# Kernel optimization log

Hardware: AMD Instinct MI355X
Metric: run time of the kernel (lower is better)

The kernel has to match this reference:

```python
import jax, jax.numpy as jnp
import numpy as np

H = 256   # hidden size
U = 10    # attention units


def _lstm_cell(xt, h, c, Wih, Whh, bih, bhh):
    # PyTorch gate order: i, f, g, o
    gates = xt @ Wih.T + h @ Whh.T + bih + bhh          # [B, 4H]
    i, f, g, o = jnp.split(gates, 4, axis=-1)
    i = jax.nn.sigmoid(i); f = jax.nn.sigmoid(f)
    g = jnp.tanh(g);       o = jax.nn.sigmoid(o)
    c = f * c + i * g
    h = o * jnp.tanh(c)
    return h, c


def setup_inputs() -> dict:
    key = jax.random.key(0)
    ks = jax.random.split(key, 12)
    B, S = 512, 256
    s = 1.0 / np.sqrt(H)
    x = jax.random.normal(ks[0], (B, S), dtype=jnp.float32)
    y = jax.random.randint(ks[1], (B, S), 0, S, dtype=jnp.int64)
    return {
        "x": x,
        "y": y,
        "enc_Wih": jax.random.uniform(ks[2], (4 * H, 1), jnp.float32, -s, s),
        "enc_Whh": jax.random.uniform(ks[3], (4 * H, H), jnp.float32, -s, s),
        "enc_bih": jax.random.uniform(ks[4], (4 * H,), jnp.float32, -s, s),
        "enc_bhh": jax.random.uniform(ks[5], (4 * H,), jnp.float32, -s, s),
        "dec_Wih": jax.random.uniform(ks[6], (4 * H, H + 1), jnp.float32, -s, s),
        "dec_Whh": jax.random.uniform(ks[7], (4 * H, H), jnp.float32, -s, s),
        "dec_bih": jax.random.uniform(ks[8], (4 * H,), jnp.float32, -s, s),
        "dec_bhh": jax.random.uniform(ks[9], (4 * H,), jnp.float32, -s, s),
        "att_W1": jax.random.uniform(ks[10], (U, H), jnp.float32, -s, s),
        "att_W2": jax.random.uniform(ks[11], (U, H), jnp.float32, -s, s),
        "att_V": jax.random.uniform(jax.random.fold_in(key, 99), (1, U), jnp.float32, -s, s),
    }


def reference(x, y, enc_Wih, enc_Whh, enc_bih, enc_bhh,
              dec_Wih, dec_Whh, dec_bih, dec_bhh,
              att_W1, att_W2, att_V):
    B, S = x.shape

    # ---- Encoder: LSTM over sequence of scalar inputs ----
    def enc_step(carry, xt):  # xt: [B, 1]
        h, c = carry
        h, c = _lstm_cell(xt, h, c, enc_Wih, enc_Whh, enc_bih, enc_bhh)
        return (h, c), h

    h0 = jnp.zeros((B, H), x.dtype)
    (hN, cN), enc_out_t = jax.lax.scan(enc_step, (h0, h0), x.T[:, :, None])
    enc_out = jnp.transpose(enc_out_t, (1, 0, 2))            # [B, S, H]

    # precompute W1 @ encoder_hidden (same math, hoisted out of loop)
    encW1 = jnp.einsum('bsh,uh->bsu', enc_out, att_W1)       # [B, S, U]

    # ---- Decoder loop (teacher forcing with ratio 1.0) ----
    def dec_step(carry, y_t):
        h, c, dec_in = carry                                  # dec_in: [B, 1]
        u = jnp.tanh(encW1 + (h @ att_W2.T)[:, None, :])      # [B, S, U]
        logits = jnp.einsum('bsu,ou->bso', u, att_V)[..., 0]  # [B, S]
        aj = jax.nn.softmax(logits, axis=1)
        di = jnp.einsum('bs,bsh->bh', aj, enc_out)            # [B, H]
        lstm_in = jnp.concatenate([di, dec_in], axis=1)       # [B, H+1]
        h, c = _lstm_cell(lstm_in, h, c, dec_Wih, dec_Whh, dec_bih, dec_bhh)
        pred = jnp.argmax(logits, axis=1)                     # [B]
        logp = jax.nn.log_softmax(logits, axis=1)
        loss_t = -jnp.mean(jnp.take_along_axis(logp, y_t[:, None], axis=1))
        dec_in_next = jnp.take_along_axis(x, y_t[:, None], axis=1)  # teacher force
        return (h, c, dec_in_next), (pred, loss_t)

    dec_in0 = jnp.zeros((B, 1), x.dtype)
    _, (preds, losses) = jax.lax.scan(dec_step, (hN, cN, dec_in0), y.T)
    outputs = preds[:, :, None].astype(jnp.int64)             # [S, B, 1]
    batch_loss = jnp.sum(losses) / B
    return outputs, batch_loss
```

## Files before the change

kernel.cpp:

```cpp
#include <hip/hip_runtime.h>
#include <cmath>

__device__ __forceinline__ double dexp_(double x) {
    x = fmin(fmax(x, -64.0), 64.0);
    double w = x * 1.4426950408889634;
    double n = rint(w);
    double u = (w - n) * 0.6931471805599453;
    double p = 1.0 + u * (1.0 + u * (0.5 + u * (1.6666666666666666e-01 +
               u * (4.1666666666666664e-02 + u * (8.3333333333333332e-03 +
               u * (1.3888888888888889e-03 + u * (1.9841269841269841e-04 +
               u * (2.4801587301587302e-05 + u * (2.7557319223985893e-06 +
               u * (2.7557319223985888e-07 + u * 2.5052108385441720e-08))))))))));
    return ldexp(p, (int)n);
}
__device__ __forceinline__ double dtanh_(double x) {
    double ax = fabs(x);
    double e = dexp_(2.0 * ax);
    double t = 1.0 - 2.0 / (e + 1.0);
    return copysign(t, x);
}
__device__ __forceinline__ double dsig_(double x) {
    return 1.0 / (1.0 + dexp_(-x));
}

__device__ __forceinline__ void fma_range(
    const float* __restrict__ wcol, int row0, const float* __restrict__ xsrc,
    int k_beg, int k_end, double& A0, double& A1, double& A2, double& A3)
{
    for (int k0 = k_beg; k0 < k_end; k0 += 8) {
        float4 w[8];
        #pragma unroll
        for (int i = 0; i < 8; ++i)
            w[i] = *(const float4*)&wcol[(row0 + k0 + i) * 1024];
        float4 xa = *(const float4*)&xsrc[k0];
        float4 xb = *(const float4*)&xsrc[k0 + 4];
        float xv[8] = {xa.x, xa.y, xa.z, xa.w, xb.x, xb.y, xb.z, xb.w};
        float s0 = 0.f, s1 = 0.f, s2 = 0.f, s3 = 0.f;
        #pragma unroll
        for (int i = 0; i < 8; ++i) {
            s0 = fmaf(w[i].x, xv[i], s0);
            s1 = fmaf(w[i].y, xv[i], s1);
            s2 = fmaf(w[i].z, xv[i], s2);
            s3 = fmaf(w[i].w, xv[i], s3);
        }
        A0 += (double)s0; A1 += (double)s1;
        A2 += (double)s2; A3 += (double)s3;
    }
}

__global__ __launch_bounds__(256) void prep_kernel(
    const float* __restrict__ eWih, const float* __restrict__ eWhh,
    const float* __restrict__ ebih, const float* __restrict__ ebhh,
    const float* __restrict__ dWih, const float* __restrict__ dWhh,
    const float* __restrict__ dbih, const float* __restrict__ dbhh,
    float* __restrict__ WencR, double* __restrict__ bencR,
    float* __restrict__ WdecR, double* __restrict__ bdecR)
{
    const int n_enc = 257 * 1024;
    const int n_dec = 513 * 1024;
    const int total = n_enc + n_dec + 2048;
    for (int idx = blockIdx.x * blockDim.x + threadIdx.x; idx < total;
         idx += gridDim.x * blockDim.x) {
        if (idx < n_enc) {
            int k = idx >> 10, c = idx & 1023;
            int j = c >> 2, g = c & 3, r = g * 256 + j;
            WencR[idx] = (k == 0) ? eWih[r] : eWhh[r * 256 + (k - 1)];
        } else if (idx < n_enc + n_dec) {
            int i2 = idx - n_enc;
            int k = i2 >> 10, c = i2 & 1023;
            int j = c >> 2, g = c & 3, r = g * 256 + j;
            WdecR[i2] = (k < 257) ? dWih[r * 257 + k] : dWhh[r * 256 + (k - 257)];
        } else {
            int c = idx - n_enc - n_dec;
            if (c < 1024) {
                int r = (c & 3) * 256 + (c >> 2);
                bencR[c] = (double)ebih[r] + (double)ebhh[r];
            } else {
                int c2 = c - 1024;
                int r = (c2 & 3) * 256 + (c2 >> 2);
                bdecR[c2] = (double)dbih[r] + (double)dbhh[r];
            }
        }
    }
}

__global__ __launch_bounds__(256, 2) void enc_fused_kernel(
    const float* __restrict__ x, const float* __restrict__ W,
    const double* __restrict__ bR, float* __restrict__ enc_out,
    float* __restrict__ c_st)
{
    __shared__ float h_lds[2][256];
    const int tid = threadIdx.x;
    const int j   = tid;
    const int b   = blockIdx.x;

    h_lds[0][j] = 0.0f;
    float c_f = 0.f;
    const double bi = bR[j * 4 + 0], bf = bR[j * 4 + 1];
    const double bg = bR[j * 4 + 2], bo = bR[j * 4 + 3];
    const float* wcol = W + j * 4;

    for (int t = 0; t < 256; ++t) {
        const int cur = t & 1, nxt = cur ^ 1;
        __syncthreads();

        double A0 = 0, A1 = 0, A2 = 0, A3 = 0;
        const float* hh = h_lds[cur];
        fma_range(wcol, 1, hh, 0, 256, A0, A1, A2, A3);
        {
            float4 w = *(const float4*)&wcol[0];
            float xv = x[b * 256 + t];
            A0 += (double)(w.x * xv); A1 += (double)(w.y * xv);
            A2 += (double)(w.z * xv); A3 += (double)(w.w * xv);
        }

        double iv = dsig_(A0 + bi);
        double fv = dsig_(A1 + bf);
        double gv = dtanh_(A2 + bg);
        double ov = dsig_(A3 + bo);
        double c = fv * (double)c_f + iv * gv;
        c_f = (float)c;
        float hv = (float)(ov * dtanh_(c));
        enc_out[(long)b * 65536 + t * 256 + j] = hv;
        h_lds[nxt][j] = hv;
    }

    c_st[(long)b * 256 + j] = c_f;
}

__global__ __launch_bounds__(256) void encW1_kernel(
    const float* __restrict__ enc_out, const float* __restrict__ W1,
    double* __restrict__ encW1d)
{
    __shared__ float sa[64][260];
    __shared__ float sw[10][257];
    const int tid = threadIdx.x;
    const int m0 = blockIdx.x * 64;
    #pragma unroll
    for (int i = 0; i < 16; ++i) {
        int idx = tid + i * 256;
        int row = idx >> 6;
        int c4 = (idx & 63) * 4;
        const float4 v = *(const float4*)&enc_out[(long)(m0 + row) * 256 + c4];
        *(float4*)&sa[row][c4] = v;
    }
    for (int i = tid; i < 2560; i += 256) sw[i >> 8][i & 255] = W1[i];
    __syncthreads();
    for (int o = tid; o < 640; o += 256) {
        int r = o / 10;
        int u = o - r * 10;
        double acc = 0.0;
        #pragma unroll 4
        for (int k = 0; k < 256; ++k)
            acc += (double)sa[r][k] * (double)sw[u][k];
        encW1d[(long)(m0 + r) * 10 + u] = acc;
    }
}

__global__ __launch_bounds__(256) void transpose_kernel(float* __restrict__ eo)
{
    __shared__ float ta[32][33], tb[32][33];
    const int tid = threadIdx.x;
    const int r   = tid >> 3;
    const int c4  = (tid & 7) * 4;
    float* base = eo + (long)blockIdx.x * 65536;

    for (int ti = 0; ti < 8; ++ti) {
        for (int tj = ti; tj < 8; ++tj) {
            float4 va = *(const float4*)&base[(ti * 32 + r) * 256 + tj * 32 + c4];
            ta[r][c4 + 0] = va.x; ta[r][c4 + 1] = va.y;
            ta[r][c4 + 2] = va.z; ta[r][c4 + 3] = va.w;
            if (tj > ti) {
                float4 vb = *(const float4*)&base[(tj * 32 + r) * 256 + ti * 32 + c4];
                tb[r][c4 + 0] = vb.x; tb[r][c4 + 1] = vb.y;
                tb[r][c4 + 2] = vb.z; tb[r][c4 + 3] = vb.w;
            }
            __syncthreads();
            {
                float4 w;
                w.x = ta[c4 + 0][r]; w.y = ta[c4 + 1][r];
                w.z = ta[c4 + 2][r]; w.w = ta[c4 + 3][r];
                *(float4*)&base[(tj * 32 + r) * 256 + ti * 32 + c4] = w;
            }
            if (tj > ti) {
                float4 w;
                w.x = tb[c4 + 0][r]; w.y = tb[c4 + 1][r];
                w.z = tb[c4 + 2][r]; w.w = tb[c4 + 3][r];
                *(float4*)&base[(ti * 32 + r) * 256 + tj * 32 + c4] = w;
            }
            __syncthreads();
        }
    }
}

__global__ __launch_bounds__(256, 2) void dec_fused_kernel(
    const double* __restrict__ encW1d, const float* __restrict__ enc_out,
    const float* __restrict__ W2, const float* __restrict__ V,
    const float* __restrict__ x, const int* __restrict__ y,
    const float* __restrict__ W, const double* __restrict__ bR,
    const float* __restrict__ c_init, float* __restrict__ logp_buf,
    float* __restrict__ out_pred)
{
    __shared__ double eW_lds[10][260];
    __shared__ float  W2_lds[10][256];
    __shared__ float h_lds[2][256];
    __shared__ float di_lds[256];
    __shared__ float e_lds[256];
    __shared__ float rcpZ_s;
    __shared__ float din_s;
    __shared__ double s_V[12];
    __shared__ double s_W2h[12];
    __shared__ double s_ld[256];
    __shared__ double s_red[4];
    __shared__ int s_redi[4];
    __shared__ double s_maxd;
    __shared__ int s_am;

    const int tid  = threadIdx.x;
    const int j    = tid;
    const int wid  = tid >> 6;
    const int lane = tid & 63;
    const int b    = blockIdx.x;

    if (tid < 10) s_V[tid] = (double)V[tid];
    for (int i = tid; i < 2560; i += 256) {
        int s = i / 10, u = i - s * 10;
        eW_lds[u][s] = encW1d[(long)b * 2560 + i];
        W2_lds[i >> 8][i & 255] = W2[i];
    }
    h_lds[0][j] = enc_out[(long)b * 65536 + j * 256 + 255];
    float c_f = c_init[(long)b * 256 + j];
    const double bi = bR[j * 4 + 0], bf = bR[j * 4 + 1];
    const double bg = bR[j * 4 + 2], bo = bR[j * 4 + 3];
    const float* wcol = W + j * 4;
    __syncthreads();

    for (int t = 0; t < 256; ++t) {
        const int cur = t & 1, nxt = cur ^ 1;
        const float* hh = h_lds[cur];

        for (int u = wid; u < 10; u += 4) {
            double p = 0.0;
            #pragma unroll
            for (int i = 0; i < 4; ++i) {
                int k = lane + i * 64;
                p += (double)W2_lds[u][k] * (double)hh[k];
            }
            #pragma unroll
            for (int off = 32; off >= 1; off >>= 1) p += __shfl_down(p, off, 64);
            if (lane == 0) s_W2h[u] = p;
        }
        __syncthreads();

        double l = 0.0;
        #pragma unroll
        for (int u = 0; u < 10; ++u) l += s_V[u] * dtanh_(eW_lds[u][j] + s_W2h[u]);
        s_ld[j] = l;

        {
            double v = l; int idx = j;
            #pragma unroll
            for (int off = 32; off >= 1; off >>= 1) {
                double v2 = __shfl_down(v, off, 64);
                int i2 = __shfl_down(idx, off, 64);
                if (v2 > v || (v2 == v && i2 < idx)) { v = v2; idx = i2; }
            }
            if (lane == 0) { s_red[wid] = v; s_redi[wid] = idx; }
        }
        __syncthreads();
        if (tid == 0) {
            double v = s_red[0]; int idx = s_redi[0];
            #pragma unroll
            for (int w2 = 1; w2 < 4; ++w2) {
                if (s_red[w2] > v || (s_red[w2] == v && s_redi[w2] < idx)) {
                    v = s_red[w2]; idx = s_redi[w2];
                }
            }
            s_maxd = v; s_am = idx;
        }
        __syncthreads();

        double e = dexp_(l - s_maxd);
        e_lds[j] = (float)e;
        {
            double v = e;
            #pragma unroll
            for (int off = 32; off >= 1; off >>= 1) v += __shfl_down(v, off, 64);
            if (lane == 0) s_red[wid] = v;
        }
        __syncthreads();
        if (tid == 0) {
            double Z = s_red[0] + s_red[1] + s_red[2] + s_red[3];
            rcpZ_s = (float)(1.0 / Z);
            out_pred[t * 512 + b] = (float)s_am;
            int yv = y[b * 256 + t];
            logp_buf[t * 512 + b] = (float)(s_ld[yv] - s_maxd - log(Z));
        } else if (tid == 1) {
            float dv = 0.0f;
            if (t > 0) { int yi = y[b * 256 + (t - 1)]; dv = x[b * 256 + yi]; }
            din_s = dv;
        }
        __syncthreads();

        {
            const float* ep = enc_out + (long)b * 65536 + j * 256;
            float acc0 = 0.f, acc1 = 0.f, acc2 = 0.f, acc3 = 0.f;
            for (int s2 = 0; s2 < 256; s2 += 4) {
                float4 v = *(const float4*)&ep[s2];
                acc0 += e_lds[s2 + 0] * v.x;
                acc1 += e_lds[s2 + 1] * v.y;
                acc2 += e_lds[s2 + 2] * v.z;
                acc3 += e_lds[s2 + 3] * v.w;
            }
            di_lds[j] = ((acc0 + acc1) + (acc2 + acc3)) * rcpZ_s;
        }
        __syncthreads();

        double A0 = 0, A1 = 0, A2 = 0, A3 = 0;

        fma_range(wcol, 0, di_lds, 0, 256, A0, A1, A2, A3);
        {
            float4 w = *(const float4*)&wcol[256 * 1024];
            float xv = din_s;
            A0 += (double)(w.x * xv); A1 += (double)(w.y * xv);
            A2 += (double)(w.z * xv); A3 += (double)(w.w * xv);
        }
        fma_range(wcol, 257, hh, 0, 256, A0, A1, A2, A3);

        double iv = dsig_(A0 + bi);
        double fv = dsig_(A1 + bf);
        double gv = dtanh_(A2 + bg);
        double ov = dsig_(A3 + bo);
        double c = fv * (double)c_f + iv * gv;
        c_f = (float)c;
        h_lds[nxt][j] = (float)(ov * dtanh_(c));
        __syncthreads();
    }
}

__global__ __launch_bounds__(256) void loss_kernel(
    const float* __restrict__ logp_buf, float* __restrict__ out)
{
    const int tid = threadIdx.x;
    double acc = 0.0;
    for (int i = tid; i < 131072; i += 256) acc += (double)logp_buf[i];
    __shared__ double s_red[4];
    const int wid = tid >> 6, lane = tid & 63;
    #pragma unroll
    for (int off = 32; off >= 1; off >>= 1) acc += __shfl_down(acc, off, 64);
    if (lane == 0) s_red[wid] = acc;
    __syncthreads();
    if (tid == 0) {
        out[131072] = (float)(-(s_red[0] + s_red[1] + s_red[2] + s_red[3])
                              / (512.0 * 512.0));
    }
}

extern "C" void kernel_launch(void* const* d_in, const int* in_sizes, int n_in,
                              void* d_out, int out_size, void* d_ws, size_t ws_size,
                              hipStream_t stream)
{
    const float* x    = (const float*)d_in[0];
    const int*   y    = (const int*)  d_in[1];
    const float* eWih = (const float*)d_in[2];
    const float* eWhh = (const float*)d_in[3];
    const float* ebih = (const float*)d_in[4];
    const float* ebhh = (const float*)d_in[5];
    const float* dWih = (const float*)d_in[6];
    const float* dWhh = (const float*)d_in[7];
    const float* dbih = (const float*)d_in[8];
    const float* dbhh = (const float*)d_in[9];
    const float* W1   = (const float*)d_in[10];
    const float* W2   = (const float*)d_in[11];
    const float* V    = (const float*)d_in[12];

    double* encW1d = (double*)d_ws;
    double* bencR  = encW1d + 1310720;
    double* bdecR  = bencR + 1024;
    float* enc_out = (float*)(bdecR + 1024);
    float* c_st    = enc_out + 33554432;
    float* hzero   = c_st + 131072;
    float* hd      = hzero + 131072;
    float* dibuf   = hd + 262144;
    float* logp    = dibuf + 131072;
    float* WencR   = logp + 131072;
    float* WdecR   = WencR + 263168;

    float* out = (float*)d_out;

    prep_kernel<<<512, 256, 0, stream>>>(eWih, eWhh, ebih, ebhh,
                                         dWih, dWhh, dbih, dbhh,
                                         WencR, bencR, WdecR, bdecR);

    enc_fused_kernel<<<512, 256, 0, stream>>>(x, WencR, bencR, enc_out, c_st);

    encW1_kernel<<<2048, 256, 0, stream>>>(enc_out, W1, encW1d);

    transpose_kernel<<<512, 256, 0, stream>>>(enc_out);

    dec_fused_kernel<<<512, 256, 0, stream>>>(encW1d, enc_out, W2, V, x, y,
                                              WdecR, bdecR, c_st, logp, out);

    loss_kernel<<<1, 256, 0, stream>>>(logp, out);
}
```

Measured before the change: 17.37 ms.

## Cut decoder block barriers and stagger second-wave block start times

```diff
diff --git a/kernel.cpp b/kernel.cpp
--- a/kernel.cpp
+++ b/kernel.cpp
@@ -46,6 +46,11 @@
         A0 += (double)s0; A1 += (double)s1;
         A2 += (double)s2; A3 += (double)s3;
     }
+}
+
+__device__ __forceinline__ void stagger_spin(long cycles) {
+    long t0 = clock64();
+    while (clock64() - t0 < cycles) {}
 }
 
 __global__ __launch_bounds__(256) void prep_kernel(
@@ -94,6 +99,8 @@
     const int j   = tid;
     const int b   = blockIdx.x;
 
+    if (b & 256) stagger_spin(12000);
+
     h_lds[0][j] = 0.0f;
     float c_f = 0.f;
     const double bi = bR[j * 4 + 0], bf = bR[j * 4 + 1];
@@ -206,21 +213,19 @@
     __shared__ float h_lds[2][256];
     __shared__ float di_lds[256];
     __shared__ float e_lds[256];
-    __shared__ float rcpZ_s;
-    __shared__ float din_s;
     __shared__ double s_V[12];
-    __shared__ double s_W2h[12];
     __shared__ double s_ld[256];
     __shared__ double s_red[4];
     __shared__ int s_redi[4];
-    __shared__ double s_maxd;
-    __shared__ int s_am;
+    __shared__ double s_red2[4];
 
     const int tid  = threadIdx.x;
     const int j    = tid;
     const int wid  = tid >> 6;
     const int lane = tid & 63;
     const int b    = blockIdx.x;
+
+    if (b & 256) stagger_spin(48000);
 
     if (tid < 10) s_V[tid] = (double)V[tid];
     for (int i = tid; i < 2560; i += 256) {
@@ -239,7 +244,9 @@
         const int cur = t & 1, nxt = cur ^ 1;
         const float* hh = h_lds[cur];
 
-        for (int u = wid; u < 10; u += 4) {
+        double w2h[10];
+        #pragma unroll
+        for (int u = 0; u < 10; ++u) {
             double p = 0.0;
             #pragma unroll
             for (int i = 0; i < 4; ++i) {
@@ -248,15 +255,13 @@
             }
             #pragma unroll
             for (int off = 32; off >= 1; off >>= 1) p += __shfl_down(p, off, 64);
-            if (lane == 0) s_W2h[u] = p;
-        }
-        __syncthreads();
+            w2h[u] = __shfl(p, 0, 64);
+        }
 
         double l = 0.0;
         #pragma unroll
-        for (int u = 0; u < 10; ++u) l += s_V[u] * dtanh_(eW_lds[u][j] + s_W2h[u]);
+        for (int u = 0; u < 10; ++u) l += s_V[u] * dtanh_(eW_lds[u][j] + w2h[u]);
         s_ld[j] = l;
-
         {
             double v = l; int idx = j;
             #pragma unroll
@@ -268,7 +273,9 @@
             if (lane == 0) { s_red[wid] = v; s_redi[wid] = idx; }
         }
         __syncthreads();
-        if (tid == 0) {
+
+        double maxd; int am;
+        {
             double v = s_red[0]; int idx = s_redi[0];
             #pragma unroll
             for (int w2 = 1; w2 < 4; ++w2) {
@@ -276,31 +283,27 @@
                     v = s_red[w2]; idx = s_redi[w2];
                 }
             }
-            s_maxd = v; s_am = idx;
-        }
-        __syncthreads();
-
-        double e = dexp_(l - s_maxd);
+            maxd = v; am = idx;
+        }
+        double e = dexp_(l - maxd);
         e_lds[j] = (float)e;
         {
             double v = e;
             #pragma unroll
             for (int off = 32; off >= 1; off >>= 1) v += __shfl_down(v, off, 64);
-            if (lane == 0) s_red[wid] = v;
+            if (lane == 0) s_red2[wid] = v;
         }
         __syncthreads();
+
+        const double Z = s_red2[0] + s_red2[1] + s_red2[2] + s_red2[3];
+        const float rcpZ = (float)(1.0 / Z);
         if (tid == 0) {
-            double Z = s_red[0] + s_red[1] + s_red[2] + s_red[3];
-            rcpZ_s = (float)(1.0 / Z);
-            out_pred[t * 512 + b] = (float)s_am;
+            out_pred[t * 512 + b] = (float)am;
             int yv = y[b * 256 + t];
-            logp_buf[t * 512 + b] = (float)(s_ld[yv] - s_maxd - log(Z));
-        } else if (tid == 1) {
-            float dv = 0.0f;
-            if (t > 0) { int yi = y[b * 256 + (t - 1)]; dv = x[b * 256 + yi]; }
-            din_s = dv;
-        }
-        __syncthreads();
+            logp_buf[t * 512 + b] = (float)(s_ld[yv] - maxd - log(Z));
+        }
+        float din = 0.0f;
+        if (t > 0) { int yi = y[b * 256 + (t - 1)]; din = x[b * 256 + yi]; }
 
         {
             const float* ep = enc_out + (long)b * 65536 + j * 256;
@@ -312,7 +315,7 @@
                 acc2 += e_lds[s2 + 2] * v.z;
                 acc3 += e_lds[s2 + 3] * v.w;
             }
-            di_lds[j] = ((acc0 + acc1) + (acc2 + acc3)) * rcpZ_s;
+            di_lds[j] = ((acc0 + acc1) + (acc2 + acc3)) * rcpZ;
         }
         __syncthreads();
 
@@ -321,9 +324,8 @@
         fma_range(wcol, 0, di_lds, 0, 256, A0, A1, A2, A3);
         {
             float4 w = *(const float4*)&wcol[256 * 1024];
-            float xv = din_s;
-            A0 += (double)(w.x * xv); A1 += (double)(w.y * xv);
-            A2 += (double)(w.z * xv); A3 += (double)(w.w * xv);
+            A0 += (double)(w.x * din); A1 += (double)(w.y * din);
+            A2 += (double)(w.z * din); A3 += (double)(w.w * din);
         }
         fma_range(wcol, 257, hh, 0, 256, A0, A1, A2, A3);
 
```

Result: slower. 18.03 ms (+3.8%).
